# Performance work log

Hardware: AMD Instinct MI355X
Metric: run time of the kernel (lower is better)

Reference implementation:

```python
import jax, jax.numpy as jnp
import numpy as np

ALPHA = 1.0  # config.cnet_alpha


def setup_inputs() -> dict:
    key = jax.random.key(0)
    k1, k2 = jax.random.split(key)
    z = jax.random.normal(k1, (8192, 2048), dtype=jnp.float32)
    centroids = jax.random.normal(k2, (512, 2048), dtype=jnp.float32)
    return {"z": z, "centroids": centroids}


def reference(z, centroids):
    # --- compute_similarity, 'EUC' branch ---
    # torch: sqrt(sum((z[None] - centroids[:, None])**2, dim=2)).T
    # computed here via the expanded quadratic form (same math, no
    # (n_clusters, bs, n_hidden) materialization):
    z_sq = jnp.sum(z * z, axis=1, keepdims=True)              # (bs, 1)
    c_sq = jnp.sum(centroids * centroids, axis=1)[None, :]    # (1, n_clusters)
    cross = jnp.einsum('bh,ch->bc', z, centroids)             # (bs, n_clusters)
    d2 = jnp.maximum(z_sq + c_sq - 2.0 * cross, 0.0)
    similarity = jnp.sqrt(d2)                                 # (bs, n_clusters)

    # --- Student-t soft assignment Q ---
    Q = jnp.power(1.0 + similarity / ALPHA, -(ALPHA + 1.0) / 2.0)
    Q = Q / jnp.nansum(Q, axis=1, keepdims=True)

    # --- target distribution P ---
    P = (Q * Q) / jnp.sum(Q, axis=0, keepdims=True)
    P = P / jnp.nansum(P, axis=1, keepdims=True)

    return jnp.stack([Q, P])  # (2, bs, n_clusters)
```

## Files before the change

kernel.cpp:

```cpp
#include <hip/hip_runtime.h>
#include <stdint.h>

#define M_ROWS 8192
#define NCLUST 512
#define KDIM   2048

#define BM 256
#define BN 256
#define BKB 128
#define KSPLIT 4
#define NKT (KDIM / KSPLIT / BKB)

typedef __attribute__((ext_vector_type(4))) int   i32x4;
typedef __attribute__((ext_vector_type(8))) int   i32x8;
typedef __attribute__((ext_vector_type(4))) float f32x4;
typedef __attribute__((ext_vector_type(8))) unsigned short u16x8;

__device__ __forceinline__ unsigned short f2bf(float f) {
    unsigned u = __float_as_uint(f);
    u += 0x7FFFu + ((u >> 16) & 1u);
    return (unsigned short)(u >> 16);
}
__device__ __forceinline__ float bf2f(unsigned short h) {
    return __uint_as_float(((unsigned)h) << 16);
}

__device__ __forceinline__ void gload_lds16(const void* g, void* l) {
    __builtin_amdgcn_global_load_lds(
        (const __attribute__((address_space(1))) void*)g,
        (__attribute__((address_space(3))) void*)l,
        16, 0, 0);
}

__global__ __launch_bounds__(256) void k_convert(
    const float* __restrict__ z, const float* __restrict__ cent,
    unsigned char* __restrict__ zb, unsigned char* __restrict__ cb,
    float* __restrict__ zsq, float* __restrict__ csq,
    float* __restrict__ colsum)
{
    int w = threadIdx.x >> 6, lane = threadIdx.x & 63;
    int row = blockIdx.x * 4 + w;

    const float* src;
    unsigned char* dst;
    float* nrm;
    int r;
    if (row < M_ROWS) { src = z + (size_t)row * KDIM; dst = zb + (size_t)row * KDIM; nrm = zsq; r = row; }
    else              { r = row - M_ROWS; src = cent + (size_t)r * KDIM; dst = cb + (size_t)r * KDIM; nrm = csq; }

    float s = 0.f;
    #pragma unroll
    for (int it = 0; it < KDIM / 256; ++it) {
        int idx = it * 256 + lane * 4;
        float4 v = *(const float4*)(src + idx);
        s += v.x * v.x + v.y * v.y + v.z * v.z + v.w * v.w;
        int p = __builtin_amdgcn_cvt_pk_fp8_f32(v.x, v.y, 0, 0);
        p     = __builtin_amdgcn_cvt_pk_fp8_f32(v.z, v.w, p, 1);
        *(int*)(dst + idx) = p;
    }
    #pragma unroll
    for (int off = 32; off; off >>= 1) s += __shfl_down(s, off);
    if (lane == 0) nrm[r] = s;

    if (blockIdx.x == 0) {
        colsum[threadIdx.x] = 0.f;
        colsum[threadIdx.x + 256] = 0.f;
    }
}

__global__ __launch_bounds__(512, 2) void k_gemm_part(
    const unsigned char* __restrict__ zb, const unsigned char* __restrict__ cb,
    unsigned short* __restrict__ parts)
{
    __shared__ unsigned char As[2][BM * BKB];
    __shared__ unsigned char Bs[2][BN * BKB];

    const int wgid = blockIdx.x;
    const int by   = wgid & 31;
    const int rest = wgid >> 5;
    const int bx   = rest & 1;
    const int bz   = rest >> 1;
    const int bRow = by * BM;
    const int bCol = bx * BN;
    const size_t kb0 = (size_t)bz * (KDIM / KSPLIT);

    const int tid  = threadIdx.x;
    const int w    = tid >> 6, lane = tid & 63;
    const int wrow = w >> 2, wcol = w & 3;

    f32x4 acc[8][4] = {};

    const int srow = lane >> 3;
    const int scol = ((lane & 7) ^ srow) * 16;
    const unsigned char* gA = zb + (size_t)(bRow + srow) * KDIM + kb0 + scol;
    const unsigned char* gB = cb + (size_t)(bCol + srow) * KDIM + kb0 + scol;

    auto stage = [&](int buf, int kt) {
        const int kb = kt * BKB;
        #pragma unroll
        for (int j = 0; j < 4; ++j) {
            const int g = w * 4 + j;
            gload_lds16(gA + (size_t)(g * 8) * KDIM + kb, &As[buf][g * 1024]);
            gload_lds16(gB + (size_t)(g * 8) * KDIM + kb, &Bs[buf][g * 1024]);
        }
    };

    const int arowb = wrow * 128 + (lane & 15);
    const int bcolb = wcol * 64 + (lane & 15);
    const int s     = lane >> 4;
    const int r7    = lane & 7;
    const int sc    = 0x7F7F7F7F;

    stage(0, 0);

    #pragma unroll
    for (int t = 0; t < NKT; ++t) {
        const int buf = t & 1;
        __builtin_amdgcn_s_barrier();
        if (t + 1 < NKT) {
            stage(buf ^ 1, t + 1);
            asm volatile("s_waitcnt vmcnt(8)" ::: "memory");
        } else {
            asm volatile("s_waitcnt vmcnt(0)" ::: "memory");
        }
        __builtin_amdgcn_sched_barrier(0);

        const unsigned char* A0 = &As[buf][0];
        const unsigned char* B0 = &Bs[buf][0];

        i32x8 bf[4];
        #pragma unroll
        for (int j = 0; j < 4; ++j) {
            const int row = bcolb + j * 16;
            const i32x4 lo = *(const i32x4*)&B0[row * BKB + ((2 * s) ^ r7) * 16];
            const i32x4 hi = *(const i32x4*)&B0[row * BKB + ((2 * s + 1) ^ r7) * 16];
            bf[j][0] = lo[0]; bf[j][1] = lo[1]; bf[j][2] = lo[2]; bf[j][3] = lo[3];
            bf[j][4] = hi[0]; bf[j][5] = hi[1]; bf[j][6] = hi[2]; bf[j][7] = hi[3];
        }

        #pragma unroll
        for (int q = 0; q < 4; ++q) {
            i32x8 af[2];
            #pragma unroll
            for (int ii = 0; ii < 2; ++ii) {
                const int row = arowb + (q * 2 + ii) * 16;
                const i32x4 lo = *(const i32x4*)&A0[row * BKB + ((2 * s) ^ r7) * 16];
                const i32x4 hi = *(const i32x4*)&A0[row * BKB + ((2 * s + 1) ^ r7) * 16];
                af[ii][0] = lo[0]; af[ii][1] = lo[1]; af[ii][2] = lo[2]; af[ii][3] = lo[3];
                af[ii][4] = hi[0]; af[ii][5] = hi[1]; af[ii][6] = hi[2]; af[ii][7] = hi[3];
            }
            asm volatile("s_waitcnt lgkmcnt(0)" ::: "memory");
            __builtin_amdgcn_sched_barrier(0);
            __builtin_amdgcn_s_setprio(1);
            #pragma unroll
            for (int ii = 0; ii < 2; ++ii)
                #pragma unroll
                for (int j = 0; j < 4; ++j)
                    acc[q * 2 + ii][j] = __builtin_amdgcn_mfma_scale_f32_16x16x128_f8f6f4(
                        af[ii], bf[j], acc[q * 2 + ii][j], 0, 0, 0, sc, 0, sc);
            __builtin_amdgcn_s_setprio(0);
            __builtin_amdgcn_sched_barrier(0);
        }
    }

    unsigned short* dst = parts + (size_t)bz * M_ROWS * NCLUST;
    const int col0 = bCol + wcol * 64 + (lane & 15);
    const int row0 = bRow + wrow * 128 + (lane >> 4) * 4;
    #pragma unroll
    for (int j = 0; j < 4; ++j) {
        const int col = col0 + j * 16;
        #pragma unroll
        for (int i = 0; i < 8; ++i)
            #pragma unroll
            for (int r = 0; r < 4; ++r)
                dst[(size_t)(row0 + i * 16 + r) * NCLUST + col] = f2bf(acc[i][j][r]);
    }
}

__global__ __launch_bounds__(256) void k_q_norm(
    const unsigned short* __restrict__ parts,
    const float* __restrict__ zsq, const float* __restrict__ csq,
    float* __restrict__ Q, float* __restrict__ colsum)
{
    __shared__ float red[4][NCLUST];
    const int tid = threadIdx.x, w = tid >> 6, lane = tid & 63;
    const size_t PSTR = (size_t)M_ROWS * NCLUST;
    float ca[8] = {0, 0, 0, 0, 0, 0, 0, 0};
    const int rbase = blockIdx.x * 32;

    float cs[8];
    {
        float4 c0 = *(const float4*)(csq + lane * 8);
        float4 c1 = *(const float4*)(csq + lane * 8 + 4);
        cs[0] = c0.x; cs[1] = c0.y; cs[2] = c0.z; cs[3] = c0.w;
        cs[4] = c1.x; cs[5] = c1.y; cs[6] = c1.z; cs[7] = c1.w;
    }

    for (int rr = 0; rr < 8; ++rr) {
        const int row = rbase + w + rr * 4;
        const size_t off = (size_t)row * NCLUST + lane * 8;
        float x[8] = {0, 0, 0, 0, 0, 0, 0, 0};
        #pragma unroll
        for (int p = 0; p < KSPLIT; ++p) {
            u16x8 v = *(const u16x8*)(parts + p * PSTR + off);
            #pragma unroll
            for (int k = 0; k < 8; ++k) x[k] += bf2f(v[k]);
        }
        const float zr = zsq[row];
        float q[8];
        float sum = 0.f;
        #pragma unroll
        for (int k = 0; k < 8; ++k) {
            q[k] = 1.0f / (1.0f + sqrtf(fmaxf(zr + cs[k] - 2.0f * x[k], 0.0f)));
            sum += q[k];
        }
        #pragma unroll
        for (int o = 32; o; o >>= 1) sum += __shfl_down(sum, o);
        sum = __shfl(sum, 0);
        const float inv = 1.0f / sum;
        float4 q0, q1;
        q0.x = q[0] * inv; q0.y = q[1] * inv; q0.z = q[2] * inv; q0.w = q[3] * inv;
        q1.x = q[4] * inv; q1.y = q[5] * inv; q1.z = q[6] * inv; q1.w = q[7] * inv;
        *(float4*)(Q + off)     = q0;
        *(float4*)(Q + off + 4) = q1;
        ca[0] += q0.x; ca[1] += q0.y; ca[2] += q0.z; ca[3] += q0.w;
        ca[4] += q1.x; ca[5] += q1.y; ca[6] += q1.z; ca[7] += q1.w;
    }
    #pragma unroll
    for (int c = 0; c < 8; ++c) red[w][lane * 8 + c] = ca[c];
    __syncthreads();
    const float t0 = red[0][tid] + red[1][tid] + red[2][tid] + red[3][tid];
    const float t1 = red[0][tid + 256] + red[1][tid + 256] + red[2][tid + 256] + red[3][tid + 256];
    atomicAdd(&colsum[tid], t0);
    atomicAdd(&colsum[tid + 256], t1);
}

__global__ __launch_bounds__(256) void k_p(
    const float* __restrict__ Q, const float* __restrict__ colsum,
    float* __restrict__ P)
{
    const int w = threadIdx.x >> 6, lane = threadIdx.x & 63;
    const int row = blockIdx.x * 4 + w;
    const float* qp = Q + (size_t)row * NCLUST;
    float4 q0 = *(const float4*)(qp + lane * 4);
    float4 q1 = *(const float4*)(qp + 256 + lane * 4);
    float4 c0 = *(const float4*)(colsum + lane * 4);
    float4 c1 = *(const float4*)(colsum + 256 + lane * 4);
    float4 p0, p1;
    p0.x = q0.x * q0.x / c0.x; p0.y = q0.y * q0.y / c0.y;
    p0.z = q0.z * q0.z / c0.z; p0.w = q0.w * q0.w / c0.w;
    p1.x = q1.x * q1.x / c1.x; p1.y = q1.y * q1.y / c1.y;
    p1.z = q1.z * q1.z / c1.z; p1.w = q1.w * q1.w / c1.w;
    float s = p0.x + p0.y + p0.z + p0.w + p1.x + p1.y + p1.z + p1.w;
    #pragma unroll
    for (int off = 32; off; off >>= 1) s += __shfl_down(s, off);
    s = __shfl(s, 0);
    const float inv = 1.0f / s;
    p0.x *= inv; p0.y *= inv; p0.z *= inv; p0.w *= inv;
    p1.x *= inv; p1.y *= inv; p1.z *= inv; p1.w *= inv;
    float* op = P + (size_t)row * NCLUST;
    *(float4*)(op + lane * 4) = p0;
    *(float4*)(op + 256 + lane * 4) = p1;
}

extern "C" void kernel_launch(void* const* d_in, const int* in_sizes, int n_in,
                              void* d_out, int out_size, void* d_ws, size_t ws_size,
                              hipStream_t stream) {
    const float* z    = (const float*)d_in[0];
    const float* cent = (const float*)d_in[1];
    float* out = (float*)d_out;

    char* ws = (char*)d_ws;
    unsigned char* zb = (unsigned char*)ws;
    unsigned char* cb = (unsigned char*)(ws + 16777216);
    float* zsq    = (float*)(ws + 17825792);
    float* csq    = (float*)(ws + 17858560);
    float* colsum = (float*)(ws + 17860608);
    unsigned short* parts = (unsigned short*)(ws + 18874368);

    float* Q = out;
    float* P = out + (size_t)M_ROWS * NCLUST;

    k_convert<<<dim3((M_ROWS + NCLUST) / 4), dim3(256), 0, stream>>>(
        z, cent, zb, cb, zsq, csq, colsum);

    k_gemm_part<<<dim3(256), dim3(512), 0, stream>>>(zb, cb, parts);

    k_q_norm<<<dim3(M_ROWS / 32), dim3(256), 0, stream>>>(
        parts, zsq, csq, Q, colsum);

    k_p<<<dim3(M_ROWS / 4), dim3(256), 0, stream>>>(Q, colsum, P);
}
```

Baseline: 65.79 us.

## Interleave next-tile global-to-LDS loads across MFMA sub-steps with per-step barriers

Splits prefetching of the next K tile into four slices, issuing one slice per MFMA sub-step instead of all at the start of the iteration. The wait for the current tile's loads moves to the first sub-step, and barriers are added inside and after each sub-step to keep waves in lockstep. The aim is to spread memory traffic evenly between matrix instructions so loads overlap better with MFMA work. In exchange it adds several workgroup barriers per K tile, which can stall waves.

Result: slower. 69.21 us (+5.2%).

```diff
diff --git a/kernel.cpp b/kernel.cpp
--- a/kernel.cpp
+++ b/kernel.cpp
@@ -95,60 +95,68 @@
     const unsigned char* gA = zb + (size_t)(bRow + srow) * KDIM + kb0 + scol;
     const unsigned char* gB = cb + (size_t)(bCol + srow) * KDIM + kb0 + scol;
 
-    auto stage = [&](int buf, int kt) {
-        const int kb = kt * BKB;
-        #pragma unroll
-        for (int j = 0; j < 4; ++j) {
-            const int g = w * 4 + j;
-            gload_lds16(gA + (size_t)(g * 8) * KDIM + kb, &As[buf][g * 1024]);
-            gload_lds16(gB + (size_t)(g * 8) * KDIM + kb, &Bs[buf][g * 1024]);
-        }
-    };
-
     const int arowb = wrow * 128 + (lane & 15);
     const int bcolb = wcol * 64 + (lane & 15);
     const int s     = lane >> 4;
     const int r7    = lane & 7;
     const int sc    = 0x7F7F7F7F;
 
-    stage(0, 0);
+    #pragma unroll
+    for (int q = 0; q < 4; ++q) {
+        const int g = w * 4 + q;
+        gload_lds16(gA + (size_t)(g * 8) * KDIM, &As[0][g * 1024]);
+        gload_lds16(gB + (size_t)(g * 8) * KDIM, &Bs[0][g * 1024]);
+    }
 
     #pragma unroll
     for (int t = 0; t < NKT; ++t) {
         const int buf = t & 1;
-        __builtin_amdgcn_s_barrier();
-        if (t + 1 < NKT) {
-            stage(buf ^ 1, t + 1);
-            asm volatile("s_waitcnt vmcnt(8)" ::: "memory");
-        } else {
-            asm volatile("s_waitcnt vmcnt(0)" ::: "memory");
-        }
-        __builtin_amdgcn_sched_barrier(0);
-
         const unsigned char* A0 = &As[buf][0];
         const unsigned char* B0 = &Bs[buf][0];
-
-        i32x8 bf[4];
-        #pragma unroll
-        for (int j = 0; j < 4; ++j) {
-            const int row = bcolb + j * 16;
-            const i32x4 lo = *(const i32x4*)&B0[row * BKB + ((2 * s) ^ r7) * 16];
-            const i32x4 hi = *(const i32x4*)&B0[row * BKB + ((2 * s + 1) ^ r7) * 16];
-            bf[j][0] = lo[0]; bf[j][1] = lo[1]; bf[j][2] = lo[2]; bf[j][3] = lo[3];
-            bf[j][4] = hi[0]; bf[j][5] = hi[1]; bf[j][6] = hi[2]; bf[j][7] = hi[3];
-        }
+        i32x8 bfr[4];
 
         #pragma unroll
         for (int q = 0; q < 4; ++q) {
+            if (t + 1 < NKT) {
+                const int g  = w * 4 + q;
+                const int kb = (t + 1) * BKB;
+                gload_lds16(gA + (size_t)(g * 8) * KDIM + kb, &As[buf ^ 1][g * 1024]);
+                gload_lds16(gB + (size_t)(g * 8) * KDIM + kb, &Bs[buf ^ 1][g * 1024]);
+            }
+
             i32x8 af[2];
-            #pragma unroll
-            for (int ii = 0; ii < 2; ++ii) {
-                const int row = arowb + (q * 2 + ii) * 16;
-                const i32x4 lo = *(const i32x4*)&A0[row * BKB + ((2 * s) ^ r7) * 16];
-                const i32x4 hi = *(const i32x4*)&A0[row * BKB + ((2 * s + 1) ^ r7) * 16];
-                af[ii][0] = lo[0]; af[ii][1] = lo[1]; af[ii][2] = lo[2]; af[ii][3] = lo[3];
-                af[ii][4] = hi[0]; af[ii][5] = hi[1]; af[ii][6] = hi[2]; af[ii][7] = hi[3];
+            if (q == 0) {
+                if (t + 1 < NKT) asm volatile("s_waitcnt vmcnt(2)" ::: "memory");
+                else             asm volatile("s_waitcnt vmcnt(0)" ::: "memory");
+                __builtin_amdgcn_s_barrier();
+                #pragma unroll
+                for (int j = 0; j < 4; ++j) {
+                    const int row = bcolb + j * 16;
+                    const i32x4 lo = *(const i32x4*)&B0[row * BKB + ((2 * s) ^ r7) * 16];
+                    const i32x4 hi = *(const i32x4*)&B0[row * BKB + ((2 * s + 1) ^ r7) * 16];
+                    bfr[j][0] = lo[0]; bfr[j][1] = lo[1]; bfr[j][2] = lo[2]; bfr[j][3] = lo[3];
+                    bfr[j][4] = hi[0]; bfr[j][5] = hi[1]; bfr[j][6] = hi[2]; bfr[j][7] = hi[3];
+                }
+                #pragma unroll
+                for (int ii = 0; ii < 2; ++ii) {
+                    const int row = arowb + ii * 16;
+                    const i32x4 lo = *(const i32x4*)&A0[row * BKB + ((2 * s) ^ r7) * 16];
+                    const i32x4 hi = *(const i32x4*)&A0[row * BKB + ((2 * s + 1) ^ r7) * 16];
+                    af[ii][0] = lo[0]; af[ii][1] = lo[1]; af[ii][2] = lo[2]; af[ii][3] = lo[3];
+                    af[ii][4] = hi[0]; af[ii][5] = hi[1]; af[ii][6] = hi[2]; af[ii][7] = hi[3];
+                }
+            } else {
+                #pragma unroll
+                for (int ii = 0; ii < 2; ++ii) {
+                    const int row = arowb + (q * 2 + ii) * 16;
+                    const i32x4 lo = *(const i32x4*)&A0[row * BKB + ((2 * s) ^ r7) * 16];
+                    const i32x4 hi = *(const i32x4*)&A0[row * BKB + ((2 * s + 1) ^ r7) * 16];
+                    af[ii][0] = lo[0]; af[ii][1] = lo[1]; af[ii][2] = lo[2]; af[ii][3] = lo[3];
+                    af[ii][4] = hi[0]; af[ii][5] = hi[1]; af[ii][6] = hi[2]; af[ii][7] = hi[3];
+                }
+                __builtin_amdgcn_s_barrier();
             }
+
             asm volatile("s_waitcnt lgkmcnt(0)" ::: "memory");
             __builtin_amdgcn_sched_barrier(0);
             __builtin_amdgcn_s_setprio(1);
@@ -157,9 +165,10 @@
                 #pragma unroll
                 for (int j = 0; j < 4; ++j)
                     acc[q * 2 + ii][j] = __builtin_amdgcn_mfma_scale_f32_16x16x128_f8f6f4(
-                        af[ii], bf[j], acc[q * 2 + ii][j], 0, 0, 0, sc, 0, sc);
+                        af[ii], bfr[j], acc[q * 2 + ii][j], 0, 0, 0, sc, 0, sc);
             __builtin_amdgcn_s_setprio(0);
             __builtin_amdgcn_sched_barrier(0);
+            __builtin_amdgcn_s_barrier();
         }
     }
 
```
